# Kernel tuning notes

Measured on AMD Instinct MI355X. Metric: run time of the kernel, lower is better.

## Reference

```python
import jax, jax.numpy as jnp
import numpy as np


def setup_inputs() -> dict:
    key = jax.random.key(0)
    k1, k2 = jax.random.split(key)
    n_points = 32768
    n_elements = 2048
    # evaluation points in [0, 1)
    x_eval = jax.random.uniform(k1, (n_points, 1), dtype=jnp.float32)
    # sorted node coordinates (monotone 1D mesh on [0, 1))
    x_full = jnp.sort(jax.random.uniform(k2, (n_elements + 1,), dtype=jnp.float32))
    return {"x_eval": x_eval, "x_full": x_full}


def reference(x_eval, x_full):
    # Vectorized over all elements at once (original loops in Python per element).
    # xa = x_full[i], xb = x_full[i+1] for each of the E = n_nodes-1 elements.
    xa = x_full[:-1]                      # [E]
    xb = x_full[1:]                       # [E]
    h = xb - xa                           # [E]
    # layer1 = relu(-x + xb); layer2 = relu(-layer1/(h+eps) + 1)
    layer1 = jax.nn.relu(xb[None, :] - x_eval)            # [P, E] (x_eval is [P,1])
    layer2 = jax.nn.relu(1.0 - layer1 / (h[None, :] + 1e-9))  # [P, E]
    N0_tilde = 1.0 - layer2               # [P, E]  (w3=-1, b3=1)
    N1_tilde = layer2                     # [P, E]  (w3=+1, b3=0)
    first = N0_tilde[:, 0:1]              # [P, 1]
    last = N1_tilde[:, -1:]               # [P, 1]
    n_nodes = x_full.shape[0]
    if n_nodes > 2:
        internal = N0_tilde[:, 1:] + N1_tilde[:, :-1] - 1.0  # [P, E-1]
        return jnp.concatenate([first, internal, last], axis=1)  # [P, n_nodes]
    return jnp.concatenate([first, last], axis=1)
```

## Files before the change

### kernel.cpp

```cpp
#include <hip/hip_runtime.h>


__global__ void scatter_hats(const float* __restrict__ x_eval,
                             const float* __restrict__ x_full,
                             float* __restrict__ out,
                             int n_points, int n_nodes) {
    extern __shared__ float s_xf[];
    for (int i = threadIdx.x; i < n_nodes; i += blockDim.x) s_xf[i] = x_full[i];
    __syncthreads();

    int p = blockIdx.x * blockDim.x + threadIdx.x;
    if (p >= n_points) return;

    float x = x_eval[p];

    int lo = 0, hi = n_nodes;
    while (lo < hi) {
        int mid = (lo + hi) >> 1;
        if (s_xf[mid] <= x) lo = mid + 1; else hi = mid;
    }
    int e0 = lo - 1;
    if (e0 < 0) e0 = 0;
    int emax = n_nodes - 2;
    if (e0 > emax) e0 = emax;

    float xa = s_xf[e0];
    float xb = s_xf[e0 + 1];
    float l1   = fmaxf(xb - x, 0.0f);
    float frac = fmaxf(1.0f - l1 / (xb - xa + 1e-9f), 0.0f);

    size_t base = (size_t)p * (size_t)n_nodes;
    out[base + e0]     = 1.0f - frac;
    out[base + e0 + 1] = frac;
}

extern "C" void kernel_launch(void* const* d_in, const int* in_sizes, int n_in,
                              void* d_out, int out_size, void* d_ws, size_t ws_size,
                              hipStream_t stream) {
    const float* x_eval = (const float*)d_in[0];
    const float* x_full = (const float*)d_in[1];
    float* out = (float*)d_out;

    int n_points = in_sizes[0];
    int n_nodes  = in_sizes[1];

    hipMemsetAsync(d_out, 0, (size_t)out_size * sizeof(float), stream);

    int block = 256;
    int grid  = (n_points + block - 1) / block;
    size_t smem = (size_t)n_nodes * sizeof(float);
    scatter_hats<<<grid, block, smem, stream>>>(x_eval, x_full, out, n_points, n_nodes);
}
```

Baseline: 256.6 us.

## Fuse zero-fill and hat scatter into one row-wise vectorized write kernel

Removes the separate memset and instead has each block write complete output rows, zeros plus the two hat values, using aligned float4 stores with scalar head and tail handling. Each block processes a contiguous chunk of rows, and all threads redundantly run the binary search for the current row. This avoids a second pass over the large output and the scattered two-element writes, at the cost of a per-row serial loop and duplicated search work.

New measurement: 273.5 us. 6.6% more time.

```diff
diff --git a/kernel.cpp b/kernel.cpp
--- a/kernel.cpp
+++ b/kernel.cpp
@@ -1,37 +1,74 @@
 #include <hip/hip_runtime.h>
+#include <stdint.h>
 
 
-__global__ void scatter_hats(const float* __restrict__ x_eval,
-                             const float* __restrict__ x_full,
-                             float* __restrict__ out,
-                             int n_points, int n_nodes) {
+__global__ __launch_bounds__(256) void hat_rows(const float* __restrict__ x_eval,
+                                                const float* __restrict__ x_full,
+                                                float* __restrict__ out,
+                                                int n_points, int n_nodes) {
     extern __shared__ float s_xf[];
     for (int i = threadIdx.x; i < n_nodes; i += blockDim.x) s_xf[i] = x_full[i];
     __syncthreads();
 
-    int p = blockIdx.x * blockDim.x + threadIdx.x;
-    if (p >= n_points) return;
+    if (n_nodes < 2) return;
 
-    float x = x_eval[p];
+    const int nb = gridDim.x;
+    const int rows_per_block = (n_points + nb - 1) / nb;
+    int r0 = blockIdx.x * rows_per_block;
+    int r1 = r0 + rows_per_block;
+    if (r1 > n_points) r1 = n_points;
 
-    int lo = 0, hi = n_nodes;
-    while (lo < hi) {
-        int mid = (lo + hi) >> 1;
-        if (s_xf[mid] <= x) lo = mid + 1; else hi = mid;
+    const int tid  = threadIdx.x;
+    const int emax = n_nodes - 2;
+
+    for (int p = r0; p < r1; ++p) {
+        float x = x_eval[p];
+
+        int lo = 0, hi = n_nodes;
+        while (lo < hi) {
+            int mid = (lo + hi) >> 1;
+            if (s_xf[mid] <= x) lo = mid + 1; else hi = mid;
+        }
+        int e0 = lo - 1;
+        e0 = e0 < 0 ? 0 : (e0 > emax ? emax : e0);
+        const int e1 = e0 + 1;
+
+        float xa = s_xf[e0];
+        float xb = s_xf[e1];
+        float l1   = fmaxf(xb - x, 0.0f);
+        float frac = fmaxf(1.0f - l1 / (xb - xa + 1e-9f), 0.0f);
+        float v0 = 1.0f - frac;
+        float v1 = frac;
+
+        float* row = out + (size_t)p * (size_t)n_nodes;
+
+        uintptr_t addr = (uintptr_t)row;
+        int h = (int)((-(addr >> 2)) & 3);
+        if (h > n_nodes) h = n_nodes;
+        int rem  = n_nodes - h;
+        int n4   = rem >> 2;
+        int tail = rem & 3;
+        int ct   = h + (n4 << 2);
+
+        if (tid < h) {
+            int c = tid;
+            row[c] = (c == e0) ? v0 : (c == e1 ? v1 : 0.0f);
+        } else if (tid - h < tail) {
+            int c = ct + (tid - h);
+            row[c] = (c == e0) ? v0 : (c == e1 ? v1 : 0.0f);
+        }
+
+        float4* __restrict__ row4 = (float4*)(row + h);
+        for (int i = tid; i < n4; i += 256) {
+            int c = h + (i << 2);
+            float4 v;
+            v.x = (c     == e0) ? v0 : (c     == e1 ? v1 : 0.0f);
+            v.y = (c + 1 == e0) ? v0 : (c + 1 == e1 ? v1 : 0.0f);
+            v.z = (c + 2 == e0) ? v0 : (c + 2 == e1 ? v1 : 0.0f);
+            v.w = (c + 3 == e0) ? v0 : (c + 3 == e1 ? v1 : 0.0f);
+            row4[i] = v;
+        }
     }
-    int e0 = lo - 1;
-    if (e0 < 0) e0 = 0;
-    int emax = n_nodes - 2;
-    if (e0 > emax) e0 = emax;
-
-    float xa = s_xf[e0];
-    float xb = s_xf[e0 + 1];
-    float l1   = fmaxf(xb - x, 0.0f);
-    float frac = fmaxf(1.0f - l1 / (xb - xa + 1e-9f), 0.0f);
-
-    size_t base = (size_t)p * (size_t)n_nodes;
-    out[base + e0]     = 1.0f - frac;
-    out[base + e0 + 1] = frac;
 }
 
 extern "C" void kernel_launch(void* const* d_in, const int* in_sizes, int n_in,
@@ -44,10 +81,9 @@
     int n_points = in_sizes[0];
     int n_nodes  = in_sizes[1];
 
-    hipMemsetAsync(d_out, 0, (size_t)out_size * sizeof(float), stream);
-
     int block = 256;
-    int grid  = (n_points + block - 1) / block;
+    int grid  = 2048;
+    if (grid > n_points) grid = n_points;
     size_t smem = (size_t)n_nodes * sizeof(float);
-    scatter_hats<<<grid, block, smem, stream>>>(x_eval, x_full, out, n_points, n_nodes);
+    hat_rows<<<grid, block, smem, stream>>>(x_eval, x_full, out, n_points, n_nodes);
 }
```
